# Performance work log

Hardware: AMD Instinct MI355X
Metric: run time of the kernel (lower is better)

Reference implementation:

```python
import jax, jax.numpy as jnp
import numpy as np

K = 7            # kernel_size
PAD = 3          # (dilation*(K-1)+1)//2
SHARE = 8        # share_planes
CIN = 512; REL = 64; COUT = 512
B = 4; H = 32; W = 32
EPS = 1e-5


def _patches(x, k, pad):
    """Reflect-pad then extract kxk local windows.
    x: [B,C,H,W] -> [B, C, k*k, H*W] (row-major kernel-offset ordering,
    matching torch Unfold / SAN's Subtraction ordering)."""
    b, c, h, w = x.shape
    xp = jnp.pad(x, ((0, 0), (0, 0), (pad, pad), (pad, pad)), mode='reflect')
    pats = jnp.stack([xp[:, :, i:i + h, j:j + w]
                      for i in range(k) for j in range(k)], axis=2)
    return pats.reshape(b, c, k * k, h * w)


def setup_inputs() -> dict:
    key = jax.random.key(0)
    ks = jax.random.split(key, 16)
    n = lambda k_, shp, s=0.05: jax.random.normal(k_, shp, dtype=jnp.float32) * s
    return {
        'x': jax.random.normal(ks[0], (B, CIN, H, W), dtype=jnp.float32),
        # 1x1 query/key/value projections
        'w1': n(ks[1], (REL, CIN)), 'b1': n(ks[2], (REL,)),
        'w2': n(ks[3], (REL, CIN)), 'b2': n(ks[4], (REL,)),
        'w3': n(ks[5], (COUT, CIN)), 'b3': n(ks[6], (COUT,)),
        # conv_p: 1x1 conv on 2-channel position map
        'wp': n(ks[7], (2, 2), 0.5), 'bp': n(ks[8], (2,)),
        # conv_w: BN(rel+2) -> ReLU -> 1x1(rel+2->rel, no bias) -> BN(rel) -> ReLU -> 1x1(rel->out/share)
        'g0': jnp.ones((REL + 2,), jnp.float32), 'be0': jnp.zeros((REL + 2,), jnp.float32),
        'm0': n(ks[9], (REL + 2,), 0.1),
        'v0': jax.random.uniform(ks[10], (REL + 2,), jnp.float32, 0.5, 1.5),
        'wcw1': n(ks[11], (REL, REL + 2)),
        'g1': jnp.ones((REL,), jnp.float32), 'be1': jnp.zeros((REL,), jnp.float32),
        'm1': n(ks[12], (REL,), 0.1),
        'v1': jax.random.uniform(ks[13], (REL,), jnp.float32, 0.5, 1.5),
        'wcw2': n(ks[14], (COUT // SHARE, REL)), 'bcw2': n(ks[15], (COUT // SHARE,)),
    }


def reference(x, w1, b1, w2, b2, w3, b3, wp, bp,
              g0, be0, m0, v0, wcw1, g1, be1, m1, v1, wcw2, bcw2):
    b, c, h, w = x.shape
    hw = h * w
    conv1x1 = lambda W_, B_, t: jnp.einsum('oc,bchw->bohw', W_, t) + B_[None, :, None, None]
    bn = lambda t, g, be, m, v: ((t - m[None, :, None, None])
                                 * (g * jax.lax.rsqrt(v + EPS))[None, :, None, None]
                                 + be[None, :, None, None])

    x1 = conv1x1(w1, b1, x)   # [B,REL,H,W]
    x2 = conv1x1(w2, b2, x)   # [B,REL,H,W]
    x3 = conv1x1(w3, b3, x)   # [B,COUT,H,W]

    # position map: channel 0 = loc_w, channel 1 = loc_h (as in source)
    lw = jnp.broadcast_to(jnp.linspace(-1.0, 1.0, w)[None, :], (h, w))
    lh = jnp.broadcast_to(jnp.linspace(-1.0, 1.0, h)[:, None], (h, w))
    p = jnp.stack([lw, lh])[None].astype(x.dtype)          # [1,2,H,W]
    p = jnp.einsum('oc,bchw->bohw', wp, p) + bp[None, :, None, None]

    # Subtraction2(x1, x2): center query minus key neighbors -> [B,REL,K*K,HW]
    sub2 = x1.reshape(b, REL, 1, hw) - _patches(x2, K, PAD)
    # Subtraction(p): center minus neighbors -> [1,2,K*K,HW], repeat over batch
    subp = p.reshape(1, 2, 1, hw) - _patches(p, K, PAD)
    subp = jnp.broadcast_to(subp, (b, 2, K * K, hw))

    t = jnp.concatenate([sub2, subp], axis=1)              # [B,REL+2,K*K,HW]
    t = jax.nn.relu(bn(t, g0, be0, m0, v0))
    t = jnp.einsum('oc,bckn->bokn', wcw1, t)               # [B,REL,K*K,HW]
    t = jax.nn.relu(bn(t, g1, be1, m1, v1))
    wgt = jnp.einsum('oc,bckn->bokn', wcw2, t) + bcw2[None, :, None, None]
    wgt = jax.nn.softmax(wgt, axis=-2)                     # softmax over K*K window dim

    # Aggregation: out[b,c,n] = sum_k wgt[b, c//SHARE, k, n] * x3_patch[b,c,k,n]
    x3p = _patches(x3, K, PAD).reshape(b, COUT // SHARE, SHARE, K * K, hw)
    out = jnp.einsum('bgskn,bgkn->bgsn', x3p, wgt)
    return out.reshape(b, COUT, h, w)
```

## Files before the change

kernel.cpp:

```cpp
#include <hip/hip_runtime.h>
#include <hip/hip_bf16.h>
#include <math.h>

typedef float f32x4 __attribute__((ext_vector_type(4)));
typedef short s16x8 __attribute__((ext_vector_type(8)));

#define KKW 49
#define HWTOT 1024
#define CIN 512
#define COUT 512

#define OFF_X1T 0
#define OFF_X2T 262144
#define OFF_X3T 524288
#define OFF_PM  2621440
#define OFF_A0  2623488
#define OFF_C0  2623554
#define OFF_W64 2623620
#define OFF_W65 2623684
#define OFF_C1V 2623748
#define OFF_W1B 2623812
#define OFF_W2B 2625860
#define OFF_W2F 2627908
#define OFF_WT  2629956
#define OFF_XT  2793796
#define WS_NEED_FLOATS 3842372ull

#define SWZ(bb)  ((bb) ^ ((((bb) >> 7) & 7) << 4))

#define GLD16(g, l) __builtin_amdgcn_global_load_lds( \
    (const __attribute__((address_space(1))) void*)(g), \
    (__attribute__((address_space(3))) void*)(l), 16, 0, 0)

__device__ __forceinline__ int refl(int m) {
    if (m < 0) m = -m;
    if (m > 31) m = 62 - m;
    return m;
}

__device__ __forceinline__ unsigned short fbf(float f) {
    unsigned u = __builtin_bit_cast(unsigned, f);
    unsigned r = u + 0x7fffu + ((u >> 16) & 1u);
    return (unsigned short)(r >> 16);
}

__device__ __forceinline__ unsigned pk2bf(float a, float b) {
    float2 f2; f2.x = a; f2.y = b;
    __hip_bfloat162 h = __float22bfloat162_rn(f2);
    union { __hip_bfloat162 h2; unsigned u; } cv;
    cv.h2 = h;
    return cv.u;
}

__device__ __forceinline__ float bf2f(unsigned short u) {
    unsigned v = (unsigned)u << 16;
    return __builtin_bit_cast(float, v);
}

__device__ __forceinline__ void setup_body(
        int tid,
        const float* __restrict__ wp, const float* __restrict__ bp,
        const float* __restrict__ g0, const float* __restrict__ be0,
        const float* __restrict__ m0, const float* __restrict__ v0,
        const float* __restrict__ wcw1,
        const float* __restrict__ g1, const float* __restrict__ be1,
        const float* __restrict__ m1, const float* __restrict__ v1,
        const float* __restrict__ wcw2,
        float* __restrict__ ws) {
    float* pm = ws + OFF_PM;
    for (int n = tid; n < HWTOT; n += 256) {
        int xx = n & 31, yy = n >> 5;
        float lw = -1.f + (2.f / 31.f) * xx;
        float lh = -1.f + (2.f / 31.f) * yy;
        pm[n * 2 + 0] = wp[0] * lw + wp[1] * lh + bp[0];
        pm[n * 2 + 1] = wp[2] * lw + wp[3] * lh + bp[1];
    }
    if (tid < 66) {
        float a = g0[tid] * rsqrtf(v0[tid] + 1e-5f);
        ws[OFF_A0 + tid] = a;
        ws[OFF_C0 + tid] = be0[tid] - m0[tid] * a;
    }
    if (tid < 64) {
        float a1c = g1[tid] * rsqrtf(v1[tid] + 1e-5f);
        ws[OFF_W64 + tid] = a1c * wcw1[tid * 66 + 64];
        ws[OFF_W65 + tid] = a1c * wcw1[tid * 66 + 65];
        ws[OFF_C1V + tid] = be1[tid] - m1[tid] * a1c;
    }
    unsigned short* w1b = (unsigned short*)(ws + OFF_W1B);
    unsigned short* w2f = (unsigned short*)(ws + OFF_W2F);
    for (int t = tid; t < 4096; t += 256) {
        int co = t >> 6, r = t & 63;
        float a1c = g1[co] * rsqrtf(v1[co] + 1e-5f);
        w1b[t] = fbf(a1c * wcw1[co * 66 + r]);
        int j = t & 7, idx = t >> 3;
        int ft = idx >> 6, l = idx & 63;
        int gt = ft >> 1, ks2 = ft & 1;
        int g = (l & 15) + gt * 16;
        int c2 = ks2 * 32 + (l >> 4) * 8 + j;
        w2f[t] = fbf(wcw2[g * 64 + c2]);
    }
}

__global__ void k_setup(const float* __restrict__ wp, const float* __restrict__ bp,
                        const float* __restrict__ g0, const float* __restrict__ be0,
                        const float* __restrict__ m0, const float* __restrict__ v0,
                        const float* __restrict__ wcw1,
                        const float* __restrict__ g1, const float* __restrict__ be1,
                        const float* __restrict__ m1, const float* __restrict__ v1,
                        const float* __restrict__ wcw2,
                        float* __restrict__ ws) {
    setup_body(threadIdx.x, wp, bp, g0, be0, m0, v0, wcw1, g1, be1, m1, v1, wcw2, ws);
}

__global__ __launch_bounds__(256) void k_prep(
        const float* __restrict__ x,
        const float* __restrict__ w1, const float* __restrict__ w2,
        const float* __restrict__ w3,
        const float* __restrict__ wp, const float* __restrict__ bp,
        const float* __restrict__ g0, const float* __restrict__ be0,
        const float* __restrict__ m0, const float* __restrict__ v0,
        const float* __restrict__ wcw1,
        const float* __restrict__ g1, const float* __restrict__ be1,
        const float* __restrict__ m1, const float* __restrict__ v1,
        const float* __restrict__ wcw2,
        float* __restrict__ ws) {
    int bid = blockIdx.x;
    int tid = threadIdx.x;
    if (bid == 296) {
        setup_body(tid, wp, bp, g0, be0, m0, v0, wcw1, g1, be1, m1, v1, wcw2, ws);
    } else if (bid < 40) {
        int mT = bid / 8, kT = bid % 8;
        char* dst = (char*)(ws + OFF_WT) + (mT * 8 + kT) * 16384;
#pragma unroll
        for (int it = 0; it < 4; ++it) {
            int item = it * 256 + tid;
            int m = item >> 3, k8 = item & 7;
            int mg = mT * 128 + m;
            const float* src;
            if (mg < 64) src = w1 + mg * CIN;
            else if (mg < 128) src = w2 + (mg - 64) * CIN;
            else src = w3 + (mg - 128) * CIN;
            int k0 = kT * 64 + k8 * 8;
            s16x8 h;
#pragma unroll
            for (int i = 0; i < 8; i++) h[i] = (short)fbf(src[k0 + i]);
            *(s16x8*)(dst + SWZ(m * 128 + k8 * 16)) = h;
        }
    } else {
        __shared__ float lds[64 * 129];
        int t = bid - 40;
        int b = t >> 6, nT = (t >> 3) & 7, kT = t & 7;
        const float* src = x + (b * CIN + kT * 64) * HWTOT + nT * 128;
#pragma unroll
        for (int it = 0; it < 8; ++it) {
            int item = it * 256 + tid;
            int kk = item >> 5, n4 = item & 31;
            float4 v = *(const float4*)(src + kk * HWTOT + n4 * 4);
            float* d = &lds[kk * 129 + n4 * 4];
            d[0] = v.x; d[1] = v.y; d[2] = v.z; d[3] = v.w;
        }
        __syncthreads();
        char* dst = (char*)(ws + OFF_XT) + ((b * 8 + nT) * 8 + kT) * 16384;
#pragma unroll
        for (int it = 0; it < 4; ++it) {
            int item = it * 256 + tid;
            int n = item >> 3, k8 = item & 7;
            s16x8 h;
#pragma unroll
            for (int i = 0; i < 8; i++) h[i] = (short)fbf(lds[(k8 * 8 + i) * 129 + n]);
            *(s16x8*)(dst + SWZ(n * 128 + k8 * 16)) = h;
        }
    }
}

__global__ __launch_bounds__(256) void k_projm(
        const float* __restrict__ b1, const float* __restrict__ b2,
        const float* __restrict__ b3, float* __restrict__ ws) {
    __shared__ __align__(16) char smem[32768];
    int tid = threadIdx.x, lane = tid & 63, wv = tid >> 6;
    int lidx = lane & 15, q = lane >> 4;
    int mT = blockIdx.x, nTT = blockIdx.y, b = blockIdx.z;
    const char* wtg = (const char*)(ws + OFF_WT) + (mT >> 1) * 8 * 16384 + (mT & 1) * 8192;
    const char* xtg = (const char*)(ws + OFF_XT) + (b * 8 + (nTT >> 1)) * 8 * 16384 + (nTT & 1) * 8192;

    f32x4 acc[4];
#pragma unroll
    for (int j = 0; j < 4; j++) acc[j] = (f32x4)0.f;

#define STAGE(kt, buf) do { \
        const char* ga_ = wtg + (kt) * 16384; \
        const char* gb_ = xtg + (kt) * 16384; \
        char* la_ = smem + (buf) * 16384; \
        char* lb_ = la_ + 8192; \
        _Pragma("unroll") \
        for (int c_ = 0; c_ < 2; c_++) { \
            GLD16(ga_ + c_ * 4096 + wv * 1024 + lane * 16, la_ + c_ * 4096 + wv * 1024); \
            GLD16(gb_ + c_ * 4096 + wv * 1024 + lane * 16, lb_ + c_ * 4096 + wv * 1024); \
        } \
    } while (0)

    STAGE(0, 0);
    __syncthreads();
    for (int kt = 0; kt < 8; kt++) {
        if (kt < 7) STAGE(kt + 1, (kt + 1) & 1);
        const char* la = smem + (kt & 1) * 16384;
        const char* lb = la + 8192;
#pragma unroll
        for (int ks = 0; ks < 2; ks++) {
            s16x8 af, bf[4];
            int kb = ks * 64 + q * 16;
            int arow = wv * 16 + lidx;
            af = *(const s16x8*)(la + SWZ(arow * 128 + kb));
#pragma unroll
            for (int f = 0; f < 4; f++) {
                int brow = f * 16 + lidx;
                bf[f] = *(const s16x8*)(lb + SWZ(brow * 128 + kb));
            }
#pragma unroll
            for (int nf = 0; nf < 4; nf++)
                acc[nf] = __builtin_amdgcn_mfma_f32_16x16x32_bf16(af, bf[nf], acc[nf], 0, 0, 0);
        }
        __syncthreads();
    }
#undef STAGE

    unsigned short* x1t = (unsigned short*)(ws + OFF_X1T);
    unsigned short* x2t = (unsigned short*)(ws + OFF_X2T);
    unsigned short* x3t = (unsigned short*)(ws + OFF_X3T);
    int mg = mT * 64 + wv * 16 + q * 4;
#pragma unroll
    for (int nf = 0; nf < 4; nf++) {
        int n = nTT * 64 + nf * 16 + lidx;
        float o[4];
        uint2 pk;
        if (mg < 64) {
#pragma unroll
            for (int r = 0; r < 4; r++)
                o[r] = ws[OFF_A0 + mg + r] * (acc[nf][r] + b1[mg + r]) + ws[OFF_C0 + mg + r];
            pk.x = pk2bf(o[0], o[1]); pk.y = pk2bf(o[2], o[3]);
            *(uint2*)(x1t + (size_t)(b * HWTOT + n) * 64 + mg) = pk;
        } else if (mg < 128) {
            int c = mg - 64;
#pragma unroll
            for (int r = 0; r < 4; r++)
                o[r] = ws[OFF_A0 + c + r] * (acc[nf][r] + b2[c + r]);
            pk.x = pk2bf(o[0], o[1]); pk.y = pk2bf(o[2], o[3]);
            *(uint2*)(x2t + (size_t)(b * HWTOT + n) * 64 + c) = pk;
        } else {
            int c = mg - 128;
#pragma unroll
            for (int r = 0; r < 4; r++)
                o[r] = acc[nf][r] + b3[c + r];
            pk.x = pk2bf(o[0], o[1]); pk.y = pk2bf(o[2], o[3]);
            *(uint2*)(x3t + (size_t)(b * HWTOT + n) * 512 + c) = pk;
        }
    }
}

__global__ __launch_bounds__(256) void k_proj(
        const float* __restrict__ x,
        const float* __restrict__ w1, const float* __restrict__ b1,
        const float* __restrict__ w2, const float* __restrict__ b2,
        const float* __restrict__ w3, const float* __restrict__ b3,
        float* __restrict__ ws) {
    __shared__ __align__(16) float As[64 * 17];
    __shared__ __align__(16) float Bs[16 * 64];
    int tid = threadIdx.x;
    int n0 = blockIdx.x * 64;
    int mT = blockIdx.y;
    int b = blockIdx.z;
    int mq = tid >> 4, nq = tid & 15;
    float acc[4][4];
#pragma unroll
    for (int i = 0; i < 4; i++)
#pragma unroll
        for (int j = 0; j < 4; j++) acc[i][j] = 0.f;

    for (int k0 = 0; k0 < CIN; k0 += 16) {
#pragma unroll
        for (int i = 0; i < 4; i++) {
            int t = tid + i * 256;
            int k = t & 15, m = t >> 4;
            int mg = mT * 64 + m;
            const float* Wrow;
            if (mg < 64) Wrow = w1 + mg * CIN;
            else if (mg < 128) Wrow = w2 + (mg - 64) * CIN;
            else Wrow = w3 + (mg - 128) * CIN;
            As[m * 17 + k] = Wrow[k0 + k];
        }
#pragma unroll
        for (int i = 0; i < 4; i++) {
            int t = tid + i * 256;
            int n = t & 63, k = t >> 6;
            Bs[k * 64 + n] = x[(b * CIN + k0 + k) * HWTOT + n0 + n];
        }
        __syncthreads();
#pragma unroll
        for (int k = 0; k < 16; k++) {
            float4 bv = *(const float4*)&Bs[k * 64 + nq * 4];
            float av[4];
#pragma unroll
            for (int i = 0; i < 4; i++) av[i] = As[(mq * 4 + i) * 17 + k];
#pragma unroll
            for (int i = 0; i < 4; i++) {
                acc[i][0] += av[i] * bv.x;
                acc[i][1] += av[i] * bv.y;
                acc[i][2] += av[i] * bv.z;
                acc[i][3] += av[i] * bv.w;
            }
        }
        __syncthreads();
    }
    unsigned short* x1t = (unsigned short*)(ws + OFF_X1T);
    unsigned short* x2t = (unsigned short*)(ws + OFF_X2T);
    unsigned short* x3t = (unsigned short*)(ws + OFF_X3T);
#pragma unroll
    for (int i = 0; i < 4; i++) {
        int mg = mT * 64 + mq * 4 + i;
        if (mg < 64) {
            float bias = b1[mg];
            float aa = ws[OFF_A0 + mg], cc = ws[OFF_C0 + mg];
#pragma unroll
            for (int j = 0; j < 4; j++) {
                int n = n0 + nq * 4 + j;
                x1t[(size_t)(b * HWTOT + n) * 64 + mg] = fbf(aa * (acc[i][j] + bias) + cc);
            }
        } else if (mg < 128) {
            int r = mg - 64;
            float bias = b2[r];
            float aa = ws[OFF_A0 + r];
#pragma unroll
            for (int j = 0; j < 4; j++) {
                int n = n0 + nq * 4 + j;
                x2t[(size_t)(b * HWTOT + n) * 64 + r] = fbf(aa * (acc[i][j] + bias));
            }
        } else {
            float bias = b3[mg - 128];
#pragma unroll
            for (int j = 0; j < 4; j++) {
                int n = n0 + nq * 4 + j;
                x3t[(size_t)(b * HWTOT + n) * 512 + (mg - 128)] = fbf(acc[i][j] + bias);
            }
        }
    }
}

__global__ __launch_bounds__(64, 4) void k_fused(
        const float* __restrict__ ws, float* __restrict__ out) {
    __shared__ __align__(16) char smem[8448];

    int lane = threadIdx.x;
    int lidx = lane & 15;
    int q = lane >> 4;

    int bid = blockIdx.x;
    int p = (bid & 7) * 512 + (bid >> 3);
    int b = p >> 10;
    int n = p & 1023;
    int y = n >> 5, x0 = n & 31;

    char* t1p = smem;
    int* nbo = (int*)(smem + 8192);

    const unsigned short* x1t = (const unsigned short*)(ws + OFF_X1T);
    const unsigned short* x2t = (const unsigned short*)(ws + OFF_X2T);
    const unsigned short* x3t = (const unsigned short*)(ws + OFF_X3T);
    const float* pm  = ws + OFF_PM;
    const unsigned short* w1b = (const unsigned short*)(ws + OFF_W1B);
    const unsigned short* w2f = (const unsigned short*)(ws + OFF_W2F);

    {
        int di = lane / 7 - 3, dj = lane % 7 - 3;
        nbo[lane] = refl(y + di) * 32 + refl(x0 + dj);
    }

    float pmn0 = pm[n * 2], pmn1 = pm[n * 2 + 1];
    float a064 = ws[OFF_A0 + 64], c064 = ws[OFF_C0 + 64];
    float a065 = ws[OFF_A0 + 65], c065 = ws[OFF_C0 + 65];
    float s64v[4], s65v[4];
    s16x8 xv[4][2];
#pragma unroll
    for (int ct = 0; ct < 4; ct++) {
        int col = lidx + 16 * ct;
        int di = col / 7 - 3, dj = col % 7 - 3;
        int nb = refl(y + di) * 32 + refl(x0 + dj);
        const unsigned short* x2r = x2t + (size_t)(b * HWTOT + nb) * 64 + q * 8;
        xv[ct][0] = *(const s16x8*)(x2r);
        xv[ct][1] = *(const s16x8*)(x2r + 32);
        float2 pmb = *(const float2*)(pm + nb * 2);
        s64v[ct] = fmaxf(fmaf(a064, pmn0 - pmb.x, c064), 0.f);
        s65v[ct] = fmaxf(fmaf(a065, pmn1 - pmb.y, c065), 0.f);
    }

    s16x8 af1[4][2];
#pragma unroll
    for (int cot = 0; cot < 4; cot++)
#pragma unroll
        for (int ks = 0; ks < 2; ks++)
            af1[cot][ks] = *(const s16x8*)(w1b + (lidx + 16 * cot) * 64 + ks * 32 + q * 8);

    const unsigned short* x1r = x1t + (size_t)(b * HWTOT + n) * 64 + q * 8;
    float x1f[2][8];
    {
        s16x8 h0 = *(const s16x8*)(x1r);
        s16x8 h1 = *(const s16x8*)(x1r + 32);
#pragma unroll
        for (int i = 0; i < 8; i++) {
            x1f[0][i] = bf2f((unsigned short)h0[i]);
            x1f[1][i] = bf2f((unsigned short)h1[i]);
        }
    }

#pragma unroll
    for (int ct = 0; ct < 4; ct++) {
        int col = lidx + 16 * ct;
        f32x4 acc1[4];
#pragma unroll
        for (int cot = 0; cot < 4; cot++) acc1[cot] = (f32x4)0.f;
#pragma unroll
        for (int ks = 0; ks < 2; ks++) {
            s16x8 v = xv[ct][ks];
            union { s16x8 v; unsigned u[4]; } bb;
#pragma unroll
            for (int w = 0; w < 4; w++)
                bb.u[w] = pk2bf(
                    fmaxf(x1f[ks][2 * w]     - bf2f((unsigned short)v[2 * w]),     0.f),
                    fmaxf(x1f[ks][2 * w + 1] - bf2f((unsigned short)v[2 * w + 1]), 0.f));
#pragma unroll
            for (int cot = 0; cot < 4; cot++)
                acc1[cot] = __builtin_amdgcn_mfma_f32_16x16x32_bf16(af1[cot][ks], bb.v, acc1[cot], 0, 0, 0);
        }
#pragma unroll
        for (int cot = 0; cot < 4; cot++) {
            f32x4 wa = *(const f32x4*)(ws + OFF_W64 + cot * 16 + q * 4);
            f32x4 wb = *(const f32x4*)(ws + OFF_W65 + cot * 16 + q * 4);
            f32x4 cc = *(const f32x4*)(ws + OFF_C1V + cot * 16 + q * 4);
            float t[4];
#pragma unroll
            for (int r = 0; r < 4; r++)
                t[r] = fmaxf(acc1[cot][r] + wa[r] * s64v[ct] + wb[r] * s65v[ct] + cc[r], 0.f);
            uint2 pk;
            pk.x = pk2bf(t[0], t[1]);
            pk.y = pk2bf(t[2], t[3]);
            int byte = col * 128 + cot * 32 + q * 8;
            *(uint2*)(t1p + SWZ(byte)) = pk;
        }
    }

    asm volatile("s_waitcnt lgkmcnt(0)" ::: "memory");
    __builtin_amdgcn_sched_barrier(0);

    s16x8 af2[4][2];
#pragma unroll
    for (int gt = 0; gt < 4; gt++)
#pragma unroll
        for (int ks2 = 0; ks2 < 2; ks2++)
            af2[gt][ks2] = *(const s16x8*)(w2f + ((gt * 2 + ks2) * 64 + lane) * 8);

    unsigned held[4][4][2];
#pragma unroll
    for (int gt = 0; gt < 4; gt++) {
        f32x4 acc2[4];
#pragma unroll
        for (int kt = 0; kt < 4; kt++) acc2[kt] = (f32x4)0.f;
#pragma unroll
        for (int kt = 0; kt < 4; kt++) {
#pragma unroll
            for (int ks2 = 0; ks2 < 2; ks2++) {
                int byte = (lidx + 16 * kt) * 128 + ks2 * 64 + q * 16;
                s16x8 a = *(const s16x8*)(t1p + SWZ(byte));
                acc2[kt] = __builtin_amdgcn_mfma_f32_16x16x32_bf16(a, af2[gt][ks2], acc2[kt], 0, 0, 0);
            }
        }
        float mx = -1e30f;
#pragma unroll
        for (int kt = 0; kt < 3; kt++)
#pragma unroll
            for (int r = 0; r < 4; r++) mx = fmaxf(mx, acc2[kt][r]);
        if (q == 0) mx = fmaxf(mx, acc2[3][0]);
        mx = fmaxf(mx, __shfl_xor(mx, 16));
        mx = fmaxf(mx, __shfl_xor(mx, 32));
        float e[4][4];
        float sum = 0.f;
#pragma unroll
        for (int kt = 0; kt < 4; kt++)
#pragma unroll
            for (int r = 0; r < 4; r++) {
                bool valid = (kt < 3) || (q == 0 && r == 0);
                float ev = valid ? exp2f((acc2[kt][r] - mx) * 1.44269504f) : 0.f;
                e[kt][r] = ev;
                sum += ev;
            }
        sum += __shfl_xor(sum, 16);
        sum += __shfl_xor(sum, 32);
        float inv = 1.f / sum;
#pragma unroll
        for (int kt = 0; kt < 4; kt++) {
            held[gt][kt][0] = pk2bf(e[kt][0] * inv, e[kt][1] * inv);
            held[gt][kt][1] = pk2bf(e[kt][2] * inv, e[kt][3] * inv);
        }
    }

#pragma unroll
    for (int gt = 0; gt < 4; gt++)
#pragma unroll
        for (int kt = 0; kt < 4; kt++) {
            int byte = (lidx + 16 * gt) * 128 + kt * 32 + q * 8;
            uint2 pk;
            pk.x = held[gt][kt][0];
            pk.y = held[gt][kt][1];
            *(uint2*)(t1p + SWZ(byte)) = pk;
        }

    asm volatile("s_waitcnt lgkmcnt(0)" ::: "memory");
    __builtin_amdgcn_sched_barrier(0);

    s16x8 wrow[7];
#pragma unroll
    for (int i = 0; i < 7; i++)
        wrow[i] = *(const s16x8*)(t1p + SWZ(lane * 128 + i * 16));

    f32x4 a30 = (f32x4)0.f, a31 = (f32x4)0.f;
    const unsigned short* x3b = x3t + (size_t)b * HWTOT * 512 + lane * 8;
#pragma unroll
    for (int k = 0; k < KKW; k++) {
        int nb = nbo[k];
        float w = bf2f((unsigned short)wrow[k >> 3][k & 7]);
        s16x8 v = *(const s16x8*)(x3b + (size_t)nb * 512);
#pragma unroll
        for (int r = 0; r < 4; r++) {
            a30[r] = fmaf(w, bf2f((unsigned short)v[r]), a30[r]);
            a31[r] = fmaf(w, bf2f((unsigned short)v[4 + r]), a31[r]);
        }
    }
    float* ob = out + ((size_t)b * COUT + lane * 8) * HWTOT + n;
#pragma unroll
    for (int i = 0; i < 4; i++) ob[i * HWTOT] = a30[i];
#pragma unroll
    for (int i = 0; i < 4; i++) ob[(i + 4) * HWTOT] = a31[i];
}

extern "C" void kernel_launch(void* const* d_in, const int* in_sizes, int n_in,
                              void* d_out, int out_size, void* d_ws, size_t ws_size,
                              hipStream_t stream) {
    const float* x = (const float*)d_in[0];
    const float* w1 = (const float*)d_in[1];
    const float* b1 = (const float*)d_in[2];
    const float* w2 = (const float*)d_in[3];
    const float* b2 = (const float*)d_in[4];
    const float* w3 = (const float*)d_in[5];
    const float* b3 = (const float*)d_in[6];
    const float* wp = (const float*)d_in[7];
    const float* bp = (const float*)d_in[8];
    const float* g0 = (const float*)d_in[9];
    const float* be0 = (const float*)d_in[10];
    const float* m0 = (const float*)d_in[11];
    const float* v0 = (const float*)d_in[12];
    const float* wcw1 = (const float*)d_in[13];
    const float* g1 = (const float*)d_in[14];
    const float* be1 = (const float*)d_in[15];
    const float* m1 = (const float*)d_in[16];
    const float* v1 = (const float*)d_in[17];
    const float* wcw2 = (const float*)d_in[18];
    float* ws = (float*)d_ws;
    float* out = (float*)d_out;

    if (ws_size >= WS_NEED_FLOATS * 4ull) {
        k_prep<<<297, 256, 0, stream>>>(x, w1, w2, w3, wp, bp, g0, be0, m0, v0,
                                        wcw1, g1, be1, m1, v1, wcw2, ws);
        k_projm<<<dim3(10, 16, 4), 256, 0, stream>>>(b1, b2, b3, ws);
    } else {
        k_setup<<<1, 256, 0, stream>>>(wp, bp, g0, be0, m0, v0, wcw1, g1, be1, m1, v1, wcw2, ws);
        k_proj<<<dim3(16, 10, 4), 256, 0, stream>>>(x, w1, b1, w2, b2, w3, b3, ws);
    }
    k_fused<<<4096, 64, 0, stream>>>(ws, out);
}
```

Baseline: 57.15 us.

## Split fused per-pixel kernel across two wavefronts per block

Adds k_fused2, which runs each pixel's fused attention-weight and aggregation pipeline with 128 threads (two wavefronts) instead of one. Each wave handles half of the neighbor column tiles and half of the share groups, with extra __syncthreads to exchange the intermediate tile and softmax weights through shared memory. The aggregation is split so each thread handles four output channels. The aim is more parallelism and latency hiding per pixel, at the cost of extra block synchronisation and more threads per block.

```diff
diff --git a/kernel.cpp b/kernel.cpp
--- a/kernel.cpp
+++ b/kernel.cpp
@@ -4,6 +4,7 @@
 
 typedef float f32x4 __attribute__((ext_vector_type(4)));
 typedef short s16x8 __attribute__((ext_vector_type(8)));
+typedef short s16x4 __attribute__((ext_vector_type(4)));
 
 #define KKW 49
 #define HWTOT 1024
@@ -343,6 +344,202 @@
             }
         }
     }
+}
+
+__global__ __launch_bounds__(128, 4) void k_fused2(
+        const float* __restrict__ ws, float* __restrict__ out) {
+    __shared__ __align__(16) char smem[8448];
+
+    int tid = threadIdx.x;
+    int lane = tid & 63;
+    int wv = tid >> 6;
+    int lidx = lane & 15;
+    int q = lane >> 4;
+
+    int bid = blockIdx.x;
+    int p = (bid & 7) * 512 + (bid >> 3);
+    int b = p >> 10;
+    int n = p & 1023;
+    int y = n >> 5, x0 = n & 31;
+
+    char* t1p = smem;
+    int* nbo = (int*)(smem + 8192);
+
+    const unsigned short* x1t = (const unsigned short*)(ws + OFF_X1T);
+    const unsigned short* x2t = (const unsigned short*)(ws + OFF_X2T);
+    const unsigned short* x3t = (const unsigned short*)(ws + OFF_X3T);
+    const float* pm  = ws + OFF_PM;
+    const unsigned short* w1b = (const unsigned short*)(ws + OFF_W1B);
+    const unsigned short* w2f = (const unsigned short*)(ws + OFF_W2F);
+
+    if (tid < 64) {
+        int di = tid / 7 - 3, dj = tid % 7 - 3;
+        nbo[tid] = refl(y + di) * 32 + refl(x0 + dj);
+    }
+
+    float pmn0 = pm[n * 2], pmn1 = pm[n * 2 + 1];
+    float a064 = ws[OFF_A0 + 64], c064 = ws[OFF_C0 + 64];
+    float a065 = ws[OFF_A0 + 65], c065 = ws[OFF_C0 + 65];
+    float s64v[2], s65v[2];
+    s16x8 xv[2][2];
+#pragma unroll
+    for (int cc = 0; cc < 2; cc++) {
+        int ct = wv * 2 + cc;
+        int col = lidx + 16 * ct;
+        int di = col / 7 - 3, dj = col % 7 - 3;
+        int nb = refl(y + di) * 32 + refl(x0 + dj);
+        const unsigned short* x2r = x2t + (size_t)(b * HWTOT + nb) * 64 + q * 8;
+        xv[cc][0] = *(const s16x8*)(x2r);
+        xv[cc][1] = *(const s16x8*)(x2r + 32);
+        float2 pmb = *(const float2*)(pm + nb * 2);
+        s64v[cc] = fmaxf(fmaf(a064, pmn0 - pmb.x, c064), 0.f);
+        s65v[cc] = fmaxf(fmaf(a065, pmn1 - pmb.y, c065), 0.f);
+    }
+
+    s16x8 af1[4][2];
+#pragma unroll
+    for (int cot = 0; cot < 4; cot++)
+#pragma unroll
+        for (int ks = 0; ks < 2; ks++)
+            af1[cot][ks] = *(const s16x8*)(w1b + (lidx + 16 * cot) * 64 + ks * 32 + q * 8);
+
+    const unsigned short* x1r = x1t + (size_t)(b * HWTOT + n) * 64 + q * 8;
+    float x1f[2][8];
+    {
+        s16x8 h0 = *(const s16x8*)(x1r);
+        s16x8 h1 = *(const s16x8*)(x1r + 32);
+#pragma unroll
+        for (int i = 0; i < 8; i++) {
+            x1f[0][i] = bf2f((unsigned short)h0[i]);
+            x1f[1][i] = bf2f((unsigned short)h1[i]);
+        }
+    }
+
+#pragma unroll
+    for (int cc = 0; cc < 2; cc++) {
+        int col = lidx + 16 * (wv * 2 + cc);
+        f32x4 acc1[4];
+#pragma unroll
+        for (int cot = 0; cot < 4; cot++) acc1[cot] = (f32x4)0.f;
+#pragma unroll
+        for (int ks = 0; ks < 2; ks++) {
+            s16x8 v = xv[cc][ks];
+            union { s16x8 v; unsigned u[4]; } bb;
+#pragma unroll
+            for (int w = 0; w < 4; w++)
+                bb.u[w] = pk2bf(
+                    fmaxf(x1f[ks][2 * w]     - bf2f((unsigned short)v[2 * w]),     0.f),
+                    fmaxf(x1f[ks][2 * w + 1] - bf2f((unsigned short)v[2 * w + 1]), 0.f));
+#pragma unroll
+            for (int cot = 0; cot < 4; cot++)
+                acc1[cot] = __builtin_amdgcn_mfma_f32_16x16x32_bf16(af1[cot][ks], bb.v, acc1[cot], 0, 0, 0);
+        }
+#pragma unroll
+        for (int cot = 0; cot < 4; cot++) {
+            f32x4 wa = *(const f32x4*)(ws + OFF_W64 + cot * 16 + q * 4);
+            f32x4 wb = *(const f32x4*)(ws + OFF_W65 + cot * 16 + q * 4);
+            f32x4 cw = *(const f32x4*)(ws + OFF_C1V + cot * 16 + q * 4);
+            float t[4];
+#pragma unroll
+            for (int r = 0; r < 4; r++)
+                t[r] = fmaxf(acc1[cot][r] + wa[r] * s64v[cc] + wb[r] * s65v[cc] + cw[r], 0.f);
+            uint2 pk;
+            pk.x = pk2bf(t[0], t[1]);
+            pk.y = pk2bf(t[2], t[3]);
+            int byte = col * 128 + cot * 32 + q * 8;
+            *(uint2*)(t1p + SWZ(byte)) = pk;
+        }
+    }
+
+    __syncthreads();
+
+    unsigned held[2][4][2];
+#pragma unroll
+    for (int gg = 0; gg < 2; gg++) {
+        int gt = wv * 2 + gg;
+        s16x8 af2[2];
+#pragma unroll
+        for (int ks2 = 0; ks2 < 2; ks2++)
+            af2[ks2] = *(const s16x8*)(w2f + ((gt * 2 + ks2) * 64 + lane) * 8);
+        f32x4 acc2[4];
+#pragma unroll
+        for (int kt = 0; kt < 4; kt++) acc2[kt] = (f32x4)0.f;
+#pragma unroll
+        for (int kt = 0; kt < 4; kt++) {
+#pragma unroll
+            for (int ks2 = 0; ks2 < 2; ks2++) {
+                int byte = (lidx + 16 * kt) * 128 + ks2 * 64 + q * 16;
+                s16x8 a = *(const s16x8*)(t1p + SWZ(byte));
+                acc2[kt] = __builtin_amdgcn_mfma_f32_16x16x32_bf16(a, af2[ks2], acc2[kt], 0, 0, 0);
+            }
+        }
+        float mx = -1e30f;
+#pragma unroll
+        for (int kt = 0; kt < 3; kt++)
+#pragma unroll
+            for (int r = 0; r < 4; r++) mx = fmaxf(mx, acc2[kt][r]);
+        if (q == 0) mx = fmaxf(mx, acc2[3][0]);
+        mx = fmaxf(mx, __shfl_xor(mx, 16));
+        mx = fmaxf(mx, __shfl_xor(mx, 32));
+        float e[4][4];
+        float sum = 0.f;
+#pragma unroll
+        for (int kt = 0; kt < 4; kt++)
+#pragma unroll
+            for (int r = 0; r < 4; r++) {
+                bool valid = (kt < 3) || (q == 0 && r == 0);
+                float ev = valid ? exp2f((acc2[kt][r] - mx) * 1.44269504f) : 0.f;
+                e[kt][r] = ev;
+                sum += ev;
+            }
+        sum += __shfl_xor(sum, 16);
+        sum += __shfl_xor(sum, 32);
+        float inv = 1.f / sum;
+#pragma unroll
+        for (int kt = 0; kt < 4; kt++) {
+            held[gg][kt][0] = pk2bf(e[kt][0] * inv, e[kt][1] * inv);
+            held[gg][kt][1] = pk2bf(e[kt][2] * inv, e[kt][3] * inv);
+        }
+    }
+
+    __syncthreads();
+
+#pragma unroll
+    for (int gg = 0; gg < 2; gg++) {
+        int gt = wv * 2 + gg;
+#pragma unroll
+        for (int kt = 0; kt < 4; kt++) {
+            int byte = (lidx + 16 * gt) * 128 + kt * 32 + q * 8;
+            uint2 pk;
+            pk.x = held[gg][kt][0];
+            pk.y = held[gg][kt][1];
+            *(uint2*)(t1p + SWZ(byte)) = pk;
+        }
+    }
+
+    __syncthreads();
+
+    int lane2 = wv * 64 + lane;
+    int g = lane2 >> 1;
+    s16x8 wrow[7];
+#pragma unroll
+    for (int i = 0; i < 7; i++)
+        wrow[i] = *(const s16x8*)(t1p + SWZ(g * 128 + i * 16));
+
+    f32x4 a30 = (f32x4)0.f;
+    const unsigned short* x3b = x3t + (size_t)b * HWTOT * 512 + lane2 * 4;
+#pragma unroll
+    for (int k = 0; k < KKW; k++) {
+        int nb = nbo[k];
+        float w = bf2f((unsigned short)wrow[k >> 3][k & 7]);
+        s16x4 v = *(const s16x4*)(x3b + (size_t)nb * 512);
+#pragma unroll
+        for (int r = 0; r < 4; r++)
+            a30[r] = fmaf(w, bf2f((unsigned short)v[r]), a30[r]);
+    }
+    float* ob = out + ((size_t)b * COUT + lane2 * 4) * HWTOT + n;
+#pragma unroll
+    for (int i = 0; i < 4; i++) ob[i * HWTOT] = a30[i];
 }
 
 __global__ __launch_bounds__(64, 4) void k_fused(
@@ -569,9 +766,10 @@
         k_prep<<<297, 256, 0, stream>>>(x, w1, w2, w3, wp, bp, g0, be0, m0, v0,
                                         wcw1, g1, be1, m1, v1, wcw2, ws);
         k_projm<<<dim3(10, 16, 4), 256, 0, stream>>>(b1, b2, b3, ws);
+        k_fused2<<<4096, 128, 0, stream>>>(ws, out);
     } else {
         k_setup<<<1, 256, 0, stream>>>(wp, bp, g0, be0, m0, v0, wcw1, g1, be1, m1, v1, wcw2, ws);
         k_proj<<<dim3(16, 10, 4), 256, 0, stream>>>(x, w1, b1, w2, b2, w3, b3, ws);
-    }
-    k_fused<<<4096, 64, 0, stream>>>(ws, out);
-}
+        k_fused<<<4096, 64, 0, stream>>>(ws, out);
+    }
+}
```

New measurement: 63.18 us. 1.11x slower.
